# Performance work log

Hardware: AMD Instinct MI355X
Metric: run time of the kernel (lower is better)

The kernel has to match this reference:

```python
import jax, jax.numpy as jnp
import numpy as np

N, M, P = 128, 16, 256   # speakers, utterances/speaker, projection dim
W, B = 10.0, -5.0        # GE2E scale/bias (abs(w)*s + b)
EPS_NORM = 1e-12
EPS_LOG = 1e-9


def setup_inputs() -> dict:
    key = jax.random.key(0)
    e = jax.random.normal(key, (N * M, P), dtype=jnp.float32)
    return {"e": e}


def _l2norm(x):
    return x / jnp.sqrt(jnp.sum(x * x, axis=-1, keepdims=True) + EPS_NORM)


def _similarity(e):
    # i_eq_j: [N*M, N], row k has 1 in column k//M
    eye = jnp.repeat(jnp.eye(N, dtype=e.dtype), M, axis=0)
    i = eye[:, :, None]                               # [N*M, N, 1]
    spk = e.reshape(N, M, P)
    cent_sum = jnp.sum(spk, axis=1)                   # [N, P] full centroid sums
    # leave-one-out subtraction only where i==j: [N*M, N, P]
    centroids = cent_sum[None, :, :] - i * e[:, None, :]
    # scale: /(m-1) for own speaker (leave-one-out), /m otherwise
    centroids = (i / (M - 1) + (1.0 - i) / M) * centroids
    e_n = _l2norm(e)                                  # [N*M, P]
    c_n = _l2norm(centroids)                          # [N*M, N, P]
    s = jnp.einsum('kp,knp->kn', e_n, c_n)            # [N*M, N]
    return s


def reference(e):
    eye = jnp.repeat(jnp.eye(N, dtype=e.dtype), M, axis=0)
    s = jnp.abs(W) * _similarity(e) + B               # [N*M, N]
    s_jij = jnp.sum(s * eye, axis=-1)                 # [N*M]
    softmax = jnp.log(jnp.sum(jnp.exp(s), axis=-1) + EPS_LOG)
    loss = jnp.mean(-s_jij + softmax)
    return (loss, s)
```

## Files before the change

kernel.cpp:

```cpp
#include <hip/hip_runtime.h>
#include <math.h>

#define N_CL 128
#define M_SPK 16
#define P_DIM 256
#define NM 2048
#define K2_BLOCKS 512
static constexpr float EPS_NORM = 1e-12f;
static constexpr float EPS_LOG  = 1e-9f;

#define WS_CENTT     0
#define WS_BLOCKLOSS 32768
#define WS_CNT       33280

__device__ __forceinline__ float waveReduceSum(float x) {
    #pragma unroll
    for (int off = 32; off > 0; off >>= 1)
        x += __shfl_xor(x, off, 64);
    return x;
}

__global__ __launch_bounds__(128)
void k1_cent(const float* __restrict__ e, float* __restrict__ ws,
             unsigned* __restrict__ cnt) {
    const int bid = blockIdx.x;
    const int n   = bid >> 1;
    const int p   = ((bid & 1) << 7) + threadIdx.x;
    const float* base = e + (size_t)n * (M_SPK * P_DIM) + p;
    float acc = 0.f;
    #pragma unroll
    for (int m = 0; m < M_SPK; ++m) acc += base[m * P_DIM];
    ws[WS_CENTT + p * N_CL + n] = acc;
    if (bid == 0 && threadIdx.x == 0) *cnt = 0u;
}

__global__ __launch_bounds__(512, 4)
void k2_fused(const float* __restrict__ e, const float* __restrict__ ws_ro,
              float* __restrict__ d_out, float* __restrict__ blockloss,
              unsigned* __restrict__ cnt) {
    const int bid  = blockIdx.x;
    const int t    = threadIdx.x;
    const int lane = t & 63;
    const int w    = t >> 6;
    const int k0   = bid * 4;
    const int nk   = bid >> 2;

    const float* centT = ws_ro + WS_CENTT;

    __shared__ float eL[4][P_DIM];
    __shared__ float pd[8][4][N_CL];
    __shared__ float caccp[8][N_CL];
    __shared__ float e2L[4], rekL[4], ownSL[4], vvL[4];
    __shared__ float expPart[8];
    __shared__ float wp[8];
    __shared__ int   lastFlag;

    {
        const float* src = e + (size_t)k0 * P_DIM;
        ((float*)eL)[t]       = src[t];
        ((float*)eL)[t + 512] = src[t + 512];
    }
    if (t == 0) lastFlag = 0;
    __syncthreads();

    if (w < 4) {
        const float* row = eL[w];
        float x0 = row[lane], x1 = row[lane + 64], x2 = row[lane + 128], x3 = row[lane + 192];
        float s2 = waveReduceSum(x0 * x0 + x1 * x1 + x2 * x2 + x3 * x3);
        if (lane == 0) { e2L[w] = s2; rekL[w] = 1.0f / sqrtf(s2 + EPS_NORM); }
    }

    float2 dot2[4] = {{0.f,0.f},{0.f,0.f},{0.f,0.f},{0.f,0.f}};
    float2 cac2 = {0.f, 0.f};
    const float2* cbase = (const float2*)centT + lane;
    const int pbase = w * 32;
    #pragma unroll 2
    for (int p0 = 0; p0 < 32; p0 += 4) {
        float2 c0 = cbase[(pbase + p0 + 0) * 64];
        float2 c1 = cbase[(pbase + p0 + 1) * 64];
        float2 c2 = cbase[(pbase + p0 + 2) * 64];
        float2 c3 = cbase[(pbase + p0 + 3) * 64];
        cac2.x = fmaf(c0.x, c0.x, cac2.x); cac2.y = fmaf(c0.y, c0.y, cac2.y);
        cac2.x = fmaf(c1.x, c1.x, cac2.x); cac2.y = fmaf(c1.y, c1.y, cac2.y);
        cac2.x = fmaf(c2.x, c2.x, cac2.x); cac2.y = fmaf(c2.y, c2.y, cac2.y);
        cac2.x = fmaf(c3.x, c3.x, cac2.x); cac2.y = fmaf(c3.y, c3.y, cac2.y);
        #pragma unroll
        for (int r = 0; r < 4; ++r) {
            float4 ev = *(const float4*)&eL[r][pbase + p0];
            dot2[r].x = fmaf(ev.x, c0.x, dot2[r].x); dot2[r].y = fmaf(ev.x, c0.y, dot2[r].y);
            dot2[r].x = fmaf(ev.y, c1.x, dot2[r].x); dot2[r].y = fmaf(ev.y, c1.y, dot2[r].y);
            dot2[r].x = fmaf(ev.z, c2.x, dot2[r].x); dot2[r].y = fmaf(ev.z, c2.y, dot2[r].y);
            dot2[r].x = fmaf(ev.w, c3.x, dot2[r].x); dot2[r].y = fmaf(ev.w, c3.y, dot2[r].y);
        }
    }
    {
        const int col0 = lane << 1;
        #pragma unroll
        for (int r = 0; r < 4; ++r)
            *(float2*)&pd[w][r][col0] = dot2[r];
        *(float2*)&caccp[w][col0] = cac2;
    }
    __syncthreads();

    const int r   = t >> 7;
    const int col = t & 127;
    float dotv = 0.f, cv = 0.f;
    #pragma unroll
    for (int ps = 0; ps < 8; ++ps) { dotv += pd[ps][r][col]; cv += caccp[ps][col]; }

    const float rek = rekL[r];
    float s;
    if (col == nk) {
        const float e2 = e2L[r];
        const float num = (dotv - e2) * (1.0f / 15.0f);
        const float hh  = (cv - 2.0f * dotv + e2) * (1.0f / 225.0f);
        s = 10.0f * (num * rek / sqrtf(hh + EPS_NORM)) - 5.0f;
        ownSL[r] = s;
    } else {
        s = 10.0f * (dotv * rek * (1.0f / sqrtf(cv + (float)(M_SPK * M_SPK) * EPS_NORM))) - 5.0f;
    }
    d_out[1 + (size_t)(k0 + r) * N_CL + col] = s;

    float psum = waveReduceSum(__expf(s));
    if (lane == 0) expPart[w] = psum;
    __syncthreads();
    if (t < 4)
        vvL[t] = __logf(expPart[2 * t] + expPart[2 * t + 1] + EPS_LOG) - ownSL[t];
    __syncthreads();

    if (t == 0) {
        float bl = vvL[0] + vvL[1] + vvL[2] + vvL[3];
        __hip_atomic_store(&blockloss[bid], bl, __ATOMIC_RELAXED, __HIP_MEMORY_SCOPE_AGENT);
        asm volatile("s_waitcnt vmcnt(0)" ::: "memory");
        unsigned old = __hip_atomic_fetch_add(cnt, 1u, __ATOMIC_RELAXED, __HIP_MEMORY_SCOPE_AGENT);
        lastFlag = (old == K2_BLOCKS - 1) ? 1 : 0;
    }
    __syncthreads();

    if (lastFlag) {
        __builtin_amdgcn_fence(__ATOMIC_ACQUIRE, "agent");
        float v = __hip_atomic_load(&blockloss[t], __ATOMIC_RELAXED, __HIP_MEMORY_SCOPE_AGENT);
        float sum = waveReduceSum(v);
        if (lane == 0) wp[w] = sum;
        __syncthreads();
        if (t == 0) {
            float tot = 0.f;
            #pragma unroll
            for (int i = 0; i < 8; ++i) tot += wp[i];
            d_out[0] = tot * (1.0f / NM);
        }
    }
}

extern "C" void kernel_launch(void* const* d_in, const int* in_sizes, int n_in,
                              void* d_out, int out_size, void* d_ws, size_t ws_size,
                              hipStream_t stream) {
    const float* e = (const float*)d_in[0];
    float* out = (float*)d_out;
    float* ws  = (float*)d_ws;
    unsigned* cnt = (unsigned*)(ws + WS_CNT);

    k1_cent<<<256, 128, 0, stream>>>(e, ws, cnt);
    k2_fused<<<K2_BLOCKS, 512, 0, stream>>>(e, ws, out, ws + WS_BLOCKLOSS, cnt);
}
```

Before: 22.60 us.

## Fuse centroid and similarity kernels into one launch with a grid-wide flag barrier

Merges the centroid-sum kernel into the main kernel. Each of 256 blocks computes a slice of the centroid sums, publishes it, sets a magic-value flag and spins until all blocks' flags are set before computing similarities. Each block now handles 8 rows instead of 4, and the final loss is reduced by block 0 after waiting on a second set of flags, replacing the atomic counter. This removes one kernel launch and the inter-kernel gap. The cost is that all 256 blocks must be co-resident, and the flags are never reset between calls, so later calls may pass the barrier early and read stale centroids.

```diff
diff --git a/kernel.cpp b/kernel.cpp
--- a/kernel.cpp
+++ b/kernel.cpp
@@ -5,13 +5,16 @@
 #define M_SPK 16
 #define P_DIM 256
 #define NM 2048
-#define K2_BLOCKS 512
+#define NBLK 256
 static constexpr float EPS_NORM = 1e-12f;
 static constexpr float EPS_LOG  = 1e-9f;
+#define MAGIC1 0x13572468u
+#define MAGIC2 0x2468ACE1u
 
-#define WS_CENTT     0
-#define WS_BLOCKLOSS 32768
-#define WS_CNT       33280
+#define WS_CENTT 0
+#define WS_BLOSS 32768
+#define WS_FLAG1 33024
+#define WS_FLAG2 33280
 
 __device__ __forceinline__ float waveReduceSum(float x) {
     #pragma unroll
@@ -20,61 +23,71 @@
     return x;
 }
 
-__global__ __launch_bounds__(128)
-void k1_cent(const float* __restrict__ e, float* __restrict__ ws,
-             unsigned* __restrict__ cnt) {
+__global__ __launch_bounds__(512, 2)
+void fused_all(const float* __restrict__ e, float* __restrict__ ws,
+               float* __restrict__ d_out) {
     const int bid = blockIdx.x;
-    const int n   = bid >> 1;
-    const int p   = ((bid & 1) << 7) + threadIdx.x;
-    const float* base = e + (size_t)n * (M_SPK * P_DIM) + p;
-    float acc = 0.f;
-    #pragma unroll
-    for (int m = 0; m < M_SPK; ++m) acc += base[m * P_DIM];
-    ws[WS_CENTT + p * N_CL + n] = acc;
-    if (bid == 0 && threadIdx.x == 0) *cnt = 0u;
-}
-
-__global__ __launch_bounds__(512, 4)
-void k2_fused(const float* __restrict__ e, const float* __restrict__ ws_ro,
-              float* __restrict__ d_out, float* __restrict__ blockloss,
-              unsigned* __restrict__ cnt) {
-    const int bid  = blockIdx.x;
     const int t    = threadIdx.x;
     const int lane = t & 63;
     const int w    = t >> 6;
-    const int k0   = bid * 4;
-    const int nk   = bid >> 2;
+    const int n    = bid >> 1;
+    const int q    = bid & 1;
+    const int k0   = bid * 8;
 
-    const float* centT = ws_ro + WS_CENTT;
+    float*    centT = ws + WS_CENTT;
+    float*    bloss = ws + WS_BLOSS;
+    unsigned* flag1 = (unsigned*)(ws + WS_FLAG1);
+    unsigned* flag2 = (unsigned*)(ws + WS_FLAG2);
 
-    __shared__ float eL[4][P_DIM];
-    __shared__ float pd[8][4][N_CL];
+    __shared__ __align__(16) float eL[8][P_DIM];
+    __shared__ float cpart[4][128];
+    __shared__ __align__(16) float pd[8][8][N_CL];
     __shared__ float caccp[8][N_CL];
-    __shared__ float e2L[4], rekL[4], ownSL[4], vvL[4];
-    __shared__ float expPart[8];
-    __shared__ float wp[8];
-    __shared__ int   lastFlag;
+    __shared__ float sL[8][N_CL];
+    __shared__ float e2L[8], rekL[8], ownSL[8], vvL[8], wpL[8];
 
     {
+        const int pl = t & 127, mg = t >> 7;
+        const float* b = e + (size_t)(n * M_SPK + mg * 4) * P_DIM + (q << 7) + pl;
+        cpart[mg][pl] = b[0] + b[P_DIM] + b[2 * P_DIM] + b[3 * P_DIM];
         const float* src = e + (size_t)k0 * P_DIM;
-        ((float*)eL)[t]       = src[t];
-        ((float*)eL)[t + 512] = src[t + 512];
+        #pragma unroll
+        for (int i = 0; i < 4; ++i)
+            ((float*)eL)[t + 512 * i] = src[t + 512 * i];
     }
-    if (t == 0) lastFlag = 0;
     __syncthreads();
-
-    if (w < 4) {
+    if (t < 128) {
+        float v = cpart[0][t] + cpart[1][t] + cpart[2][t] + cpart[3][t];
+        __hip_atomic_store(&centT[(size_t)((q << 7) | t) * N_CL + n], v,
+                           __ATOMIC_RELAXED, __HIP_MEMORY_SCOPE_AGENT);
+    }
+    {
         const float* row = eL[w];
         float x0 = row[lane], x1 = row[lane + 64], x2 = row[lane + 128], x3 = row[lane + 192];
         float s2 = waveReduceSum(x0 * x0 + x1 * x1 + x2 * x2 + x3 * x3);
         if (lane == 0) { e2L[w] = s2; rekL[w] = 1.0f / sqrtf(s2 + EPS_NORM); }
     }
+    asm volatile("s_waitcnt vmcnt(0)" ::: "memory");
+    __syncthreads();
+    if (t == 0)
+        __hip_atomic_store(&flag1[bid], MAGIC1, __ATOMIC_RELAXED, __HIP_MEMORY_SCOPE_AGENT);
 
-    float2 dot2[4] = {{0.f,0.f},{0.f,0.f},{0.f,0.f},{0.f,0.f}};
-    float2 cac2 = {0.f, 0.f};
+    for (;;) {
+        unsigned f = (t < NBLK)
+            ? __hip_atomic_load(&flag1[t], __ATOMIC_RELAXED, __HIP_MEMORY_SCOPE_AGENT)
+            : MAGIC1;
+        if (__syncthreads_and(f == MAGIC1)) break;
+        __builtin_amdgcn_s_sleep(8);
+    }
+    __builtin_amdgcn_fence(__ATOMIC_ACQUIRE, "agent");
+
+    float2 dot2[8];
+    #pragma unroll
+    for (int r = 0; r < 8; ++r) dot2[r] = make_float2(0.f, 0.f);
+    float2 cac2 = make_float2(0.f, 0.f);
     const float2* cbase = (const float2*)centT + lane;
     const int pbase = w * 32;
-    #pragma unroll 2
+    #pragma unroll 4
     for (int p0 = 0; p0 < 32; p0 += 4) {
         float2 c0 = cbase[(pbase + p0 + 0) * 64];
         float2 c1 = cbase[(pbase + p0 + 1) * 64];
@@ -85,7 +98,7 @@
         cac2.x = fmaf(c2.x, c2.x, cac2.x); cac2.y = fmaf(c2.y, c2.y, cac2.y);
         cac2.x = fmaf(c3.x, c3.x, cac2.x); cac2.y = fmaf(c3.y, c3.y, cac2.y);
         #pragma unroll
-        for (int r = 0; r < 4; ++r) {
+        for (int r = 0; r < 8; ++r) {
             float4 ev = *(const float4*)&eL[r][pbase + p0];
             dot2[r].x = fmaf(ev.x, c0.x, dot2[r].x); dot2[r].y = fmaf(ev.x, c0.y, dot2[r].y);
             dot2[r].x = fmaf(ev.y, c1.x, dot2[r].x); dot2[r].y = fmaf(ev.y, c1.y, dot2[r].y);
@@ -96,57 +109,73 @@
     {
         const int col0 = lane << 1;
         #pragma unroll
-        for (int r = 0; r < 4; ++r)
+        for (int r = 0; r < 8; ++r)
             *(float2*)&pd[w][r][col0] = dot2[r];
         *(float2*)&caccp[w][col0] = cac2;
     }
     __syncthreads();
 
-    const int r   = t >> 7;
-    const int col = t & 127;
-    float dotv = 0.f, cv = 0.f;
-    #pragma unroll
-    for (int ps = 0; ps < 8; ++ps) { dotv += pd[ps][r][col]; cv += caccp[ps][col]; }
-
-    const float rek = rekL[r];
-    float s;
-    if (col == nk) {
-        const float e2 = e2L[r];
-        const float num = (dotv - e2) * (1.0f / 15.0f);
-        const float hh  = (cv - 2.0f * dotv + e2) * (1.0f / 225.0f);
-        s = 10.0f * (num * rek / sqrtf(hh + EPS_NORM)) - 5.0f;
-        ownSL[r] = s;
-    } else {
-        s = 10.0f * (dotv * rek * (1.0f / sqrtf(cv + (float)(M_SPK * M_SPK) * EPS_NORM))) - 5.0f;
-    }
-    d_out[1 + (size_t)(k0 + r) * N_CL + col] = s;
-
-    float psum = waveReduceSum(__expf(s));
-    if (lane == 0) expPart[w] = psum;
-    __syncthreads();
-    if (t < 4)
-        vvL[t] = __logf(expPart[2 * t] + expPart[2 * t + 1] + EPS_LOG) - ownSL[t];
-    __syncthreads();
-
-    if (t == 0) {
-        float bl = vvL[0] + vvL[1] + vvL[2] + vvL[3];
-        __hip_atomic_store(&blockloss[bid], bl, __ATOMIC_RELAXED, __HIP_MEMORY_SCOPE_AGENT);
-        asm volatile("s_waitcnt vmcnt(0)" ::: "memory");
-        unsigned old = __hip_atomic_fetch_add(cnt, 1u, __ATOMIC_RELAXED, __HIP_MEMORY_SCOPE_AGENT);
-        lastFlag = (old == K2_BLOCKS - 1) ? 1 : 0;
+    {
+        const int col = t & 127;
+        const int rb  = (t >> 7) * 2;
+        float cv = 0.f;
+        #pragma unroll
+        for (int ps = 0; ps < 8; ++ps) cv += caccp[ps][col];
+        const float sco = 1.0f / sqrtf(cv + (float)(M_SPK * M_SPK) * EPS_NORM);
+        #pragma unroll
+        for (int rr = 0; rr < 2; ++rr) {
+            const int r = rb + rr;
+            float dv = 0.f;
+            #pragma unroll
+            for (int ps = 0; ps < 8; ++ps) dv += pd[ps][r][col];
+            float s;
+            if (col == n) {
+                const float e2  = e2L[r];
+                const float num = (dv - e2) * (1.0f / 15.0f);
+                const float hh  = (cv - 2.0f * dv + e2) * (1.0f / 225.0f);
+                s = 10.0f * (num * rekL[r] / sqrtf(hh + EPS_NORM)) - 5.0f;
+                ownSL[r] = s;
+            } else {
+                s = 10.0f * (dv * rekL[r] * sco) - 5.0f;
+            }
+            sL[r][col] = s;
+            d_out[1 + (size_t)(k0 + r) * N_CL + col] = s;
+        }
     }
     __syncthreads();
+    {
+        float ex = __expf(sL[w][lane]) + __expf(sL[w][lane + 64]);
+        float rs = waveReduceSum(ex);
+        if (lane == 0) vvL[w] = __logf(rs + EPS_LOG) - ownSL[w];
+    }
+    __syncthreads();
+    if (t == 0) {
+        float bl = 0.f;
+        #pragma unroll
+        for (int i = 0; i < 8; ++i) bl += vvL[i];
+        __hip_atomic_store(&bloss[bid], bl, __ATOMIC_RELAXED, __HIP_MEMORY_SCOPE_AGENT);
+        asm volatile("s_waitcnt vmcnt(0)" ::: "memory");
+        __hip_atomic_store(&flag2[bid], MAGIC2, __ATOMIC_RELAXED, __HIP_MEMORY_SCOPE_AGENT);
+    }
 
-    if (lastFlag) {
-        __builtin_amdgcn_fence(__ATOMIC_ACQUIRE, "agent");
-        float v = __hip_atomic_load(&blockloss[t], __ATOMIC_RELAXED, __HIP_MEMORY_SCOPE_AGENT);
+    if (bid == 0) {
+        for (;;) {
+            unsigned f = (t < NBLK)
+                ? __hip_atomic_load(&flag2[t], __ATOMIC_RELAXED, __HIP_MEMORY_SCOPE_AGENT)
+                : MAGIC2;
+            if (__syncthreads_and(f == MAGIC2)) break;
+            __builtin_amdgcn_s_sleep(8);
+        }
+        float v = (t < NBLK)
+            ? __hip_atomic_load(&bloss[t], __ATOMIC_RELAXED, __HIP_MEMORY_SCOPE_AGENT)
+            : 0.f;
         float sum = waveReduceSum(v);
-        if (lane == 0) wp[w] = sum;
+        if (lane == 0) wpL[w] = sum;
         __syncthreads();
         if (t == 0) {
             float tot = 0.f;
             #pragma unroll
-            for (int i = 0; i < 8; ++i) tot += wp[i];
+            for (int i = 0; i < 8; ++i) tot += wpL[i];
             d_out[0] = tot * (1.0f / NM);
         }
     }
@@ -156,10 +185,5 @@
                               void* d_out, int out_size, void* d_ws, size_t ws_size,
                               hipStream_t stream) {
     const float* e = (const float*)d_in[0];
-    float* out = (float*)d_out;
-    float* ws  = (float*)d_ws;
-    unsigned* cnt = (unsigned*)(ws + WS_CNT);
-
-    k1_cent<<<256, 128, 0, stream>>>(e, ws, cnt);
-    k2_fused<<<K2_BLOCKS, 512, 0, stream>>>(e, ws, out, ws + WS_BLOCKLOSS, cnt);
+    fused_all<<<NBLK, 512, 0, stream>>>(e, (float*)d_ws, (float*)d_out);
 }
```

Result: slower. 29.88 us (+32.2%).
